# Kernel optimization log

Hardware: AMD Instinct MI355X
Metric: run time of the kernel (lower is better)

The kernel has to match this reference:

```python
import jax, jax.numpy as jnp
import numpy as np
import math

B, L, D, K = 16, 8192, 256, 320
BN_EPS = 1e-5


def setup_inputs() -> dict:
    key = jax.random.key(0)
    k1, k2, k3, k4 = jax.random.split(key, 4)
    x = jax.random.normal(k1, (B, L, D), dtype=jnp.float32)
    bn_weight = 1.0 + 0.1 * jax.random.normal(k2, (D,), dtype=jnp.float32)
    bn_bias = 0.1 * jax.random.normal(k3, (D,), dtype=jnp.float32)
    # xavier_uniform for Embedding(numCodes, codeDim)
    a = math.sqrt(6.0 / (K + D))
    codebook = jax.random.uniform(k4, (K, D), minval=-a, maxval=a, dtype=jnp.float32)
    return {"x": x, "bn_weight": bn_weight, "bn_bias": bn_bias, "codebook": codebook}


def batchnorm1d(x, weight, bias):
    # BatchNorm1d in training mode: stats over (batch, length) per channel,
    # biased variance for normalization (matches torch).
    mean = jnp.mean(x, axis=(0, 1))
    var = jnp.var(x, axis=(0, 1))
    return (x - mean) * jax.lax.rsqrt(var + BN_EPS) * weight + bias


def reference(x, bn_weight, bn_bias, codebook):
    xb = batchnorm1d(x, bn_weight, bn_bias)            # [B, L, D]
    flat = xb.reshape(-1, D)                           # [B*L, D]
    # squared euclidean distance (same argmin as torch.cdist)
    d2 = (jnp.sum(flat * flat, axis=-1, keepdims=True)
          - 2.0 * flat @ codebook.T
          + jnp.sum(codebook * codebook, axis=-1))     # [B*L, K]
    indices = jnp.argmin(d2, axis=-1)                  # [B*L]
    codes = codebook[indices].reshape(B, L, D)         # gather nearest codes
    return codes, indices.reshape(B, L, 1)
```

## Files before the change

kernel.cpp:

```cpp
#include <hip/hip_runtime.h>
#include <hip/hip_bf16.h>

#define NROW 131072
#define D 256
#define K 320
#define BN_EPS 1e-5f
#define FIXSCALE 16777216.0f

typedef _Float16 half8 __attribute__((ext_vector_type(8)));
typedef float f32x4 __attribute__((ext_vector_type(4)));


__global__ __launch_bounds__(256) void k_zero(unsigned long long* __restrict__ acc) {
  acc[threadIdx.x] = 0ull;
  acc[256 + threadIdx.x] = 0ull;
}

__global__ __launch_bounds__(256) void k_stats_partial(const float* __restrict__ x,
                                                       unsigned long long* __restrict__ acc) {
  const int d = threadIdx.x;
  const int blk = blockIdx.x;
  const float* p = x + (size_t)blk * 256 * D + d;
  float s = 0.f, q = 0.f;
  #pragma unroll 4
  for (int r = 0; r < 256; ++r) {
    float v = p[(size_t)r * D];
    s += v;
    q = fmaf(v, v, q);
  }
  long long si = llrintf(s * FIXSCALE);
  long long qi = llrintf(q * FIXSCALE);
  atomicAdd(&acc[d],       (unsigned long long)si);
  atomicAdd(&acc[256 + d], (unsigned long long)qi);
}

__global__ __launch_bounds__(256) void k_stats_final(const unsigned long long* __restrict__ acc,
                                                     const float* __restrict__ cb,
                                                     float* __restrict__ meanb,
                                                     float* __restrict__ rsb,
                                                     float* __restrict__ cnorm) {
  const int t = threadIdx.x;
  if (blockIdx.x == 0) {
    double s = (double)(long long)acc[t]       / (double)FIXSCALE;
    double q = (double)(long long)acc[256 + t] / (double)FIXSCALE;
    double mean = s / (double)NROW;
    double var  = q / (double)NROW - mean * mean;
    meanb[t] = (float)mean;
    rsb[t]   = (float)(1.0 / sqrt(var + (double)BN_EPS));
  } else {
    for (int code = t; code < K; code += 256) {
      const float* c = cb + (size_t)code * D;
      float s = 0.f;
      for (int dd = 0; dd < D; ++dd) s = fmaf(c[dd], c[dd], s);
      cnorm[code] = s;
    }
  }
}

__global__ __launch_bounds__(64) void k_cbprep(const float* __restrict__ cb,
                                               _Float16* __restrict__ cbx) {
  const int nt = blockIdx.x;
  const int ks = blockIdx.y;
  const int l  = threadIdx.x;
  const int code = nt * 16 + (l & 15);
  const int d0 = ks * 32 + (l >> 4) * 8;
  const float* src = cb + (size_t)code * D + d0;
  const size_t bh = ((size_t)(nt * 2 + 0) * 8 + ks) * 512 + l * 8;
  const size_t bl = ((size_t)(nt * 2 + 1) * 8 + ks) * 512 + l * 8;
  #pragma unroll
  for (int j = 0; j < 8; ++j) {
    float v = src[j];
    _Float16 h = (_Float16)v;
    _Float16 lo = (_Float16)(v - (float)h);
    cbx[bh + j] = h;
    cbx[bl + j] = lo;
  }
}

__global__ __launch_bounds__(512, 4) void k_main(const float* __restrict__ x,
                                                 const float* __restrict__ w,
                                                 const float* __restrict__ bias,
                                                 const float* __restrict__ cb,
                                                 const float* __restrict__ meanb,
                                                 const float* __restrict__ rsb,
                                                 const float* __restrict__ cnorm,
                                                 const _Float16* __restrict__ cbx,
                                                 float* __restrict__ out) {
  __shared__ _Float16 Bbuf[2][16384];
  __shared__ float sxs[128];
  __shared__ int bsel[128];

  const int t = threadIdx.x;
  const int lane = t & 63;
  const int wv = t >> 6;
  const int c15 = lane & 15;
  const int g = lane >> 4;
  const int row0 = (int)blockIdx.x * 128;

  float4 s0, s1, s2, s3;
  const char* stg_src = (const char*)cbx + (size_t)t * 16;
#define ISSUE(c) {                                                  \
    const char* p_ = stg_src + (size_t)(c) * 32768;                 \
    s0 = *(const float4*)(p_);                                      \
    s1 = *(const float4*)(p_ + 8192);                               \
    s2 = *(const float4*)(p_ + 16384);                              \
    s3 = *(const float4*)(p_ + 24576);                              \
  }
#define WRITE(b) {                                                  \
    char* q_ = (char*)Bbuf[b] + t * 16;                             \
    *(float4*)(q_)         = s0;                                    \
    *(float4*)(q_ + 8192)  = s1;                                    \
    *(float4*)(q_ + 16384) = s2;                                    \
    *(float4*)(q_ + 24576) = s3;                                    \
  }

  ISSUE(0);

  half8 ah[8], al[8];
  float accq = 0.f;
  {
    const int arow = row0 + wv * 16 + c15;
    const int dbase = g * 8;
    const float* xp = x + (size_t)arow * D + dbase;
    #pragma unroll
    for (int ks = 0; ks < 8; ++ks) {
      const int d0 = dbase + ks * 32;
      float4 xa = *(const float4*)(xp + ks * 32);
      float4 xb2 = *(const float4*)(xp + ks * 32 + 4);
      float4 m0 = *(const float4*)(meanb + d0);
      float4 m1 = *(const float4*)(meanb + d0 + 4);
      float4 r0 = *(const float4*)(rsb + d0);
      float4 r1 = *(const float4*)(rsb + d0 + 4);
      float4 w0 = *(const float4*)(w + d0);
      float4 w1 = *(const float4*)(w + d0 + 4);
      float4 b0 = *(const float4*)(bias + d0);
      float4 b1 = *(const float4*)(bias + d0 + 4);
      float o0 = ((xa.x - m0.x) * r0.x) * w0.x + b0.x;
      float o1 = ((xa.y - m0.y) * r0.y) * w0.y + b0.y;
      float o2 = ((xa.z - m0.z) * r0.z) * w0.z + b0.z;
      float o3 = ((xa.w - m0.w) * r0.w) * w0.w + b0.w;
      float o4 = ((xb2.x - m1.x) * r1.x) * w1.x + b1.x;
      float o5 = ((xb2.y - m1.y) * r1.y) * w1.y + b1.y;
      float o6 = ((xb2.z - m1.z) * r1.z) * w1.z + b1.z;
      float o7 = ((xb2.w - m1.w) * r1.w) * w1.w + b1.w;
      accq = fmaf(o0, o0, accq);
      accq = fmaf(o1, o1, accq);
      accq = fmaf(o2, o2, accq);
      accq = fmaf(o3, o3, accq);
      accq = fmaf(o4, o4, accq);
      accq = fmaf(o5, o5, accq);
      accq = fmaf(o6, o6, accq);
      accq = fmaf(o7, o7, accq);
      _Float16 h;
      h = (_Float16)o0; ah[ks][0] = h; al[ks][0] = (_Float16)(o0 - (float)h);
      h = (_Float16)o1; ah[ks][1] = h; al[ks][1] = (_Float16)(o1 - (float)h);
      h = (_Float16)o2; ah[ks][2] = h; al[ks][2] = (_Float16)(o2 - (float)h);
      h = (_Float16)o3; ah[ks][3] = h; al[ks][3] = (_Float16)(o3 - (float)h);
      h = (_Float16)o4; ah[ks][4] = h; al[ks][4] = (_Float16)(o4 - (float)h);
      h = (_Float16)o5; ah[ks][5] = h; al[ks][5] = (_Float16)(o5 - (float)h);
      h = (_Float16)o6; ah[ks][6] = h; al[ks][6] = (_Float16)(o6 - (float)h);
      h = (_Float16)o7; ah[ks][7] = h; al[ks][7] = (_Float16)(o7 - (float)h);
    }
  }
  {
    float v1 = accq + __shfl_xor(accq, 16);
    float sxrow = v1 + __shfl_xor(v1, 32);
    if (lane < 16) sxs[wv * 16 + lane] = sxrow;
  }

  WRITE(0);
  ISSUE(1);
  __syncthreads();

  float bv[4];
  int   bix[4];
  #pragma unroll
  for (int r = 0; r < 4; ++r) { bv[r] = 3.4e38f; bix[r] = 0x7fffffff; }

  float sxr[4];
  #pragma unroll
  for (int r = 0; r < 4; ++r) sxr[r] = sxs[wv * 16 + g * 4 + r];

  for (int c = 0; c < 10; ++c) {
    const _Float16* bb = Bbuf[c & 1] + lane * 8;
    f32x4 acc[2];
    #pragma unroll
    for (int tt = 0; tt < 2; ++tt) {
      acc[tt] = (f32x4){0.f, 0.f, 0.f, 0.f};
      #pragma unroll
      for (int ks = 0; ks < 8; ++ks) {
        half8 bh = *(const half8*)(bb + ((tt * 2 + 0) * 8 + ks) * 512);
        half8 bl = *(const half8*)(bb + ((tt * 2 + 1) * 8 + ks) * 512);
        acc[tt] = __builtin_amdgcn_mfma_f32_16x16x32_f16(ah[ks], bh, acc[tt], 0, 0, 0);
        acc[tt] = __builtin_amdgcn_mfma_f32_16x16x32_f16(ah[ks], bl, acc[tt], 0, 0, 0);
        acc[tt] = __builtin_amdgcn_mfma_f32_16x16x32_f16(al[ks], bh, acc[tt], 0, 0, 0);
      }
    }
    #pragma unroll
    for (int tt = 0; tt < 2; ++tt) {
      const int code = c * 32 + tt * 16 + c15;
      const float cn = cnorm[code];
      #pragma unroll
      for (int r = 0; r < 4; ++r) {
        const float d2 = (sxr[r] - 2.0f * acc[tt][r]) + cn;
        if (d2 < bv[r] || (d2 == bv[r] && code < bix[r])) { bv[r] = d2; bix[r] = code; }
      }
    }
    if (c < 9) {
      WRITE((c + 1) & 1);
      if (c + 2 < 10) ISSUE(c + 2);
      __syncthreads();
    }
  }

  #pragma unroll
  for (int off = 8; off >= 1; off >>= 1) {
    #pragma unroll
    for (int r = 0; r < 4; ++r) {
      const float ov = __shfl_xor(bv[r], off);
      const int   oi = __shfl_xor(bix[r], off);
      if (ov < bv[r] || (ov == bv[r] && oi < bix[r])) { bv[r] = ov; bix[r] = oi; }
    }
  }
  if (c15 == 0) {
    #pragma unroll
    for (int r = 0; r < 4; ++r) {
      const int row = wv * 16 + g * 4 + r;
      bsel[row] = bix[r];
      out[(size_t)NROW * D + row0 + row] = (float)bix[r];
    }
  }
  __syncthreads();

  {
    const int lr = t >> 2;
    const int q = t & 3;
    const int code = bsel[lr];
    const float* cp = cb + (size_t)code * D;
    float* op = out + (size_t)(row0 + lr) * D;
    #pragma unroll
    for (int e = 0; e < 16; ++e) {
      *(float4*)(op + e * 16 + q * 4) = *(const float4*)(cp + e * 16 + q * 4);
    }
  }
#undef ISSUE
#undef WRITE
}

extern "C" void kernel_launch(void* const* d_in, const int* in_sizes, int n_in,
                              void* d_out, int out_size, void* d_ws, size_t ws_size,
                              hipStream_t stream) {
  const float* x    = (const float*)d_in[0];
  const float* w    = (const float*)d_in[1];
  const float* bias = (const float*)d_in[2];
  const float* cb   = (const float*)d_in[3];
  float* out = (float*)d_out;

  unsigned long long* acc = (unsigned long long*)d_ws;
  float* meanb = (float*)((char*)d_ws + 4096);
  float* rsb   = meanb + 256;
  float* cnorm = rsb + 256;
  _Float16* cbx = (_Float16*)((char*)d_ws + 8192);

  k_zero<<<1, 256, 0, stream>>>(acc);
  k_cbprep<<<dim3(20, 8), 64, 0, stream>>>(cb, cbx);
  k_stats_partial<<<512, 256, 0, stream>>>(x, acc);
  k_stats_final<<<2, 256, 0, stream>>>(acc, cb, meanb, rsb, cnorm);
  k_main<<<NROW / 128, 512, 0, stream>>>(x, w, bias, cb, meanb, rsb, cnorm, cbx, out);
}
```

Baseline: 154.2 us.

## Halve main kernel tile to 64 rows and 16-code stages with earlier LDS staging

The distance/argmin kernel now processes 64 rows per 256-thread block instead of 128 rows per 512-thread block. It streams the codebook in 20 chunks of 16 codes, with half-size LDS double buffers. The write of the next chunk into LDS and the global prefetch of the one after are moved to the start of each iteration, so they overlap with the MFMA work, leaving one barrier per iteration. This gives more, smaller blocks for occupancy and scheduling flexibility. In exchange, each block re-reads the full split-fp16 codebook for half as many rows, doubling codebook traffic, and the kernel runs twice as many barriers.

```diff
diff --git a/kernel.cpp b/kernel.cpp
--- a/kernel.cpp
+++ b/kernel.cpp
@@ -77,41 +77,41 @@
   }
 }
 
-__global__ __launch_bounds__(512, 4) void k_main(const float* __restrict__ x,
-                                                 const float* __restrict__ w,
-                                                 const float* __restrict__ bias,
-                                                 const float* __restrict__ cb,
-                                                 const float* __restrict__ meanb,
-                                                 const float* __restrict__ rsb,
-                                                 const float* __restrict__ cnorm,
-                                                 const _Float16* __restrict__ cbx,
-                                                 float* __restrict__ out) {
-  __shared__ _Float16 Bbuf[2][16384];
-  __shared__ float sxs[128];
-  __shared__ int bsel[128];
+__global__ __launch_bounds__(256) void k_main(const float* __restrict__ x,
+                                              const float* __restrict__ w,
+                                              const float* __restrict__ bias,
+                                              const float* __restrict__ cb,
+                                              const float* __restrict__ meanb,
+                                              const float* __restrict__ rsb,
+                                              const float* __restrict__ cnorm,
+                                              const _Float16* __restrict__ cbx,
+                                              float* __restrict__ out) {
+  __shared__ _Float16 Bbuf[2][8192];
+  __shared__ float sxs[64];
+  __shared__ int bsel[64];
 
   const int t = threadIdx.x;
   const int lane = t & 63;
   const int wv = t >> 6;
   const int c15 = lane & 15;
   const int g = lane >> 4;
-  const int row0 = (int)blockIdx.x * 128;
+  const int row0 = (int)blockIdx.x * 64;
 
   float4 s0, s1, s2, s3;
   const char* stg_src = (const char*)cbx + (size_t)t * 16;
 #define ISSUE(c) {                                                  \
-    const char* p_ = stg_src + (size_t)(c) * 32768;                 \
+    const char* p_ = stg_src + (size_t)(c) * 16384;                 \
     s0 = *(const float4*)(p_);                                      \
-    s1 = *(const float4*)(p_ + 8192);                               \
-    s2 = *(const float4*)(p_ + 16384);                              \
-    s3 = *(const float4*)(p_ + 24576);                              \
+    s1 = *(const float4*)(p_ + 4096);                               \
+    s2 = *(const float4*)(p_ + 8192);                               \
+    s3 = *(const float4*)(p_ + 12288);                              \
   }
 #define WRITE(b) {                                                  \
-    char* q_ = (char*)Bbuf[b] + t * 16;                             \
+    char* q_ = (char*)Bbuf[(b)] + t * 16;                           \
     *(float4*)(q_)         = s0;                                    \
-    *(float4*)(q_ + 8192)  = s1;                                    \
-    *(float4*)(q_ + 16384) = s2;                                    \
-    *(float4*)(q_ + 24576) = s3;                                    \
+    *(float4*)(q_ + 4096)  = s1;                                    \
+    *(float4*)(q_ + 8192)  = s2;                                    \
+    *(float4*)(q_ + 12288) = s3;                                    \
   }
 
   ISSUE(0);
@@ -143,14 +143,10 @@
       float o5 = ((xb2.y - m1.y) * r1.y) * w1.y + b1.y;
       float o6 = ((xb2.z - m1.z) * r1.z) * w1.z + b1.z;
       float o7 = ((xb2.w - m1.w) * r1.w) * w1.w + b1.w;
-      accq = fmaf(o0, o0, accq);
-      accq = fmaf(o1, o1, accq);
-      accq = fmaf(o2, o2, accq);
-      accq = fmaf(o3, o3, accq);
-      accq = fmaf(o4, o4, accq);
-      accq = fmaf(o5, o5, accq);
-      accq = fmaf(o6, o6, accq);
-      accq = fmaf(o7, o7, accq);
+      accq = fmaf(o0, o0, accq); accq = fmaf(o1, o1, accq);
+      accq = fmaf(o2, o2, accq); accq = fmaf(o3, o3, accq);
+      accq = fmaf(o4, o4, accq); accq = fmaf(o5, o5, accq);
+      accq = fmaf(o6, o6, accq); accq = fmaf(o7, o7, accq);
       _Float16 h;
       h = (_Float16)o0; ah[ks][0] = h; al[ks][0] = (_Float16)(o0 - (float)h);
       h = (_Float16)o1; ah[ks][1] = h; al[ks][1] = (_Float16)(o1 - (float)h);
@@ -162,14 +158,15 @@
       h = (_Float16)o7; ah[ks][7] = h; al[ks][7] = (_Float16)(o7 - (float)h);
     }
   }
+
+  WRITE(0);
+  ISSUE(1);
+
   {
     float v1 = accq + __shfl_xor(accq, 16);
     float sxrow = v1 + __shfl_xor(v1, 32);
     if (lane < 16) sxs[wv * 16 + lane] = sxrow;
   }
-
-  WRITE(0);
-  ISSUE(1);
   __syncthreads();
 
   float bv[4];
@@ -181,36 +178,30 @@
   #pragma unroll
   for (int r = 0; r < 4; ++r) sxr[r] = sxs[wv * 16 + g * 4 + r];
 
-  for (int c = 0; c < 10; ++c) {
-    const _Float16* bb = Bbuf[c & 1] + lane * 8;
-    f32x4 acc[2];
-    #pragma unroll
-    for (int tt = 0; tt < 2; ++tt) {
-      acc[tt] = (f32x4){0.f, 0.f, 0.f, 0.f};
+  for (int c = 0; c < 20; ++c) {
+    if (c + 1 < 20) WRITE((c + 1) & 1);
+    if (c + 2 < 20) ISSUE(c + 2);
+
+    {
+      const _Float16* bb = Bbuf[c & 1] + lane * 8;
+      f32x4 acc = (f32x4){0.f, 0.f, 0.f, 0.f};
       #pragma unroll
       for (int ks = 0; ks < 8; ++ks) {
-        half8 bh = *(const half8*)(bb + ((tt * 2 + 0) * 8 + ks) * 512);
-        half8 bl = *(const half8*)(bb + ((tt * 2 + 1) * 8 + ks) * 512);
-        acc[tt] = __builtin_amdgcn_mfma_f32_16x16x32_f16(ah[ks], bh, acc[tt], 0, 0, 0);
-        acc[tt] = __builtin_amdgcn_mfma_f32_16x16x32_f16(ah[ks], bl, acc[tt], 0, 0, 0);
-        acc[tt] = __builtin_amdgcn_mfma_f32_16x16x32_f16(al[ks], bh, acc[tt], 0, 0, 0);
+        half8 bh = *(const half8*)(bb + ks * 512);
+        half8 bl = *(const half8*)(bb + 4096 + ks * 512);
+        acc = __builtin_amdgcn_mfma_f32_16x16x32_f16(ah[ks], bh, acc, 0, 0, 0);
+        acc = __builtin_amdgcn_mfma_f32_16x16x32_f16(ah[ks], bl, acc, 0, 0, 0);
+        acc = __builtin_amdgcn_mfma_f32_16x16x32_f16(al[ks], bh, acc, 0, 0, 0);
       }
-    }
-    #pragma unroll
-    for (int tt = 0; tt < 2; ++tt) {
-      const int code = c * 32 + tt * 16 + c15;
+      const int code = c * 16 + c15;
       const float cn = cnorm[code];
       #pragma unroll
       for (int r = 0; r < 4; ++r) {
-        const float d2 = (sxr[r] - 2.0f * acc[tt][r]) + cn;
+        const float d2 = (sxr[r] - 2.0f * acc[r]) + cn;
         if (d2 < bv[r] || (d2 == bv[r] && code < bix[r])) { bv[r] = d2; bix[r] = code; }
       }
     }
-    if (c < 9) {
-      WRITE((c + 1) & 1);
-      if (c + 2 < 10) ISSUE(c + 2);
-      __syncthreads();
-    }
+    if (c < 19) __syncthreads();
   }
 
   #pragma unroll
@@ -266,5 +257,5 @@
   k_cbprep<<<dim3(20, 8), 64, 0, stream>>>(cb, cbx);
   k_stats_partial<<<512, 256, 0, stream>>>(x, acc);
   k_stats_final<<<2, 256, 0, stream>>>(acc, cb, meanb, rsb, cnorm);
-  k_main<<<NROW / 128, 512, 0, stream>>>(x, w, bias, cb, meanb, rsb, cnorm, cbx, out);
-}
+  k_main<<<NROW / 64, 256, 0, stream>>>(x, w, bias, cb, meanb, rsb, cnorm, cbx, out);
+}
```

Result: faster. 146.4 us (-5.1%).
